# Kernel optimization log

Measured on AMD Instinct MI355X. Metric: run time of the kernel, lower is better.

The kernel has to match this reference:

```python
import jax, jax.numpy as jnp
import numpy as np

HIDDEN = 1024
HEADS = 16
HEAD_DIM = HIDDEN // HEADS


def setup_inputs() -> dict:
    key = jax.random.key(0)
    ks = jax.random.split(key, 12)
    B, S, D = 4, 2048, HIDDEN
    scale = 1.0 / np.sqrt(D)
    inp = {
        'q': jax.random.normal(ks[0], (B, S, D), jnp.float32),
        'k': jax.random.normal(ks[1], (B, S, D), jnp.float32),
        'v': jax.random.normal(ks[2], (B, S, D), jnp.float32),
        'Wq': jax.random.normal(ks[3], (D, D), jnp.float32) * scale,
        'bq': jnp.zeros((D,), jnp.float32),
        'Wk': jax.random.normal(ks[4], (D, D), jnp.float32) * scale,
        'bk': jnp.zeros((D,), jnp.float32),
        'Wv': jax.random.normal(ks[5], (D, D), jnp.float32) * scale,
        'bv': jnp.zeros((D,), jnp.float32),
        'Wo': jax.random.normal(ks[6], (D, D), jnp.float32) * scale,
        'bo': jnp.zeros((D,), jnp.float32),
    }
    return inp


def reference(q, k, v, Wq, bq, Wk, bk, Wv, bv, Wo, bo):
    B, S, D = q.shape
    H, Dh = HEADS, HEAD_DIM
    # QKV projections (weights stored as [in, out])
    Q = q @ Wq + bq
    K = k @ Wk + bk
    V = v @ Wv + bv
    # [B, H, S, Dh]
    Qh = Q.reshape(B, S, H, Dh).transpose(0, 2, 1, 3)
    Kh = K.reshape(B, S, H, Dh).transpose(0, 2, 1, 3)
    Vh = V.reshape(B, S, H, Dh).transpose(0, 2, 1, 3)
    # scaled dot-product attention, full [B,H,S,S] scores as in source
    scores = jnp.einsum('bhqd,bhkd->bhqk', Qh, Kh) / jnp.sqrt(jnp.float32(Dh))
    attn = jax.nn.softmax(scores, axis=-1)
    ctx = jnp.einsum('bhqk,bhkd->bhqd', attn, Vh)
    out = ctx.transpose(0, 2, 1, 3).reshape(B, S, D)
    return out @ Wo + bo
```

## Files before the change

kernel.cpp:

```cpp
#include <hip/hip_runtime.h>
#include <hip/hip_bf16.h>

#define HID 1024
#define NH 16
#define DH 64
#define NB 4
#define SQ 2048

typedef __bf16 bf16x8 __attribute__((ext_vector_type(8)));
typedef __bf16 bf16x2 __attribute__((ext_vector_type(2)));
typedef float f32x4 __attribute__((ext_vector_type(4)));
typedef float f32x16 __attribute__((ext_vector_type(16)));
typedef unsigned int u32x4 __attribute__((ext_vector_type(4)));

static __device__ __forceinline__ unsigned pkbf(float a, float b) {
  bf16x2 t; t[0] = (__bf16)a; t[1] = (__bf16)b;
  return __builtin_bit_cast(unsigned, t);
}

static __device__ __forceinline__ void gload16(const void* g, void* l) {
  __builtin_amdgcn_global_load_lds(
      (const __attribute__((address_space(1))) unsigned int*)g,
      (__attribute__((address_space(3))) unsigned int*)l, 16, 0, 0);
}

static __device__ __forceinline__ int xcd_swz(int lin, int nwg) {
  return (lin & 7) * (nwg >> 3) + (lin >> 3);
}

__global__ __launch_bounds__(256) void transpose_wf4_kernel(
    const float* __restrict__ Wq, const float* __restrict__ Wk,
    const float* __restrict__ Wv, const float* __restrict__ Wo,
    __bf16* __restrict__ Wcatf, __bf16* __restrict__ Wof) {
  const int which = blockIdx.z;
  const float* W = which == 0 ? Wq : (which == 1 ? Wk : (which == 2 ? Wv : Wo));
  __bf16* Wf = which == 3 ? Wof : Wcatf + (size_t)which * HID * HID;
  const int nblk = blockIdx.x, kt = blockIdx.y;
  const int tid = threadIdx.x, lane = tid & 63, wid = tid >> 6;
  const int fr = lane & 15, g = lane >> 4;
#pragma unroll
  for (int c = 0; c < 2; ++c) {
    const int wn_i = wid + c * 4;
    const int wn = wn_i >> 2, i = wn_i & 3;
    const int n = nblk * 128 + wn * 64 + i * 16 + fr;
    const int kb = kt * 32 + g * 8;
    bf16x8 v;
#pragma unroll
    for (int e = 0; e < 8; ++e)
      v[e] = (__bf16)W[(size_t)(kb + e) * HID + n];
    *reinterpret_cast<bf16x8*>(
        &Wf[(size_t)(nblk * 32 + kt) * 4096 + wn * 2048 + i * 512 + lane * 8]) = v;
  }
}

__global__ __launch_bounds__(256) void cvt_a_kernel(
    const float* __restrict__ q, const float* __restrict__ k,
    const float* __restrict__ v, __bf16* __restrict__ Abf) {
  const int which = blockIdx.y;
  const float* src = which == 0 ? q : (which == 1 ? k : v);
  __bf16* dst = Abf + (size_t)which * ((size_t)NB * SQ * HID);
  const size_t base = ((size_t)blockIdx.x * 256 + threadIdx.x) * 16;
  float4 f0 = *reinterpret_cast<const float4*>(src + base);
  float4 f1 = *reinterpret_cast<const float4*>(src + base + 4);
  float4 f2 = *reinterpret_cast<const float4*>(src + base + 8);
  float4 f3 = *reinterpret_cast<const float4*>(src + base + 12);
  u32x4 w0, w1;
  w0[0] = pkbf(f0.x, f0.y); w0[1] = pkbf(f0.z, f0.w);
  w0[2] = pkbf(f1.x, f1.y); w0[3] = pkbf(f1.z, f1.w);
  w1[0] = pkbf(f2.x, f2.y); w1[1] = pkbf(f2.z, f2.w);
  w1[2] = pkbf(f3.x, f3.y); w1[3] = pkbf(f3.z, f3.w);
  *reinterpret_cast<u32x4*>(dst + base) = w0;
  *reinterpret_cast<u32x4*>(dst + base + 8) = w1;
}

__global__ __launch_bounds__(256) void gemm_qkv_kernel(
    const __bf16* __restrict__ Abf, const __bf16* __restrict__ Wcatf,
    const float* __restrict__ bq, const float* __restrict__ bk,
    const float* __restrict__ bv, __bf16* __restrict__ Qh,
    __bf16* __restrict__ Kh, __bf16* __restrict__ Vt, float qscale) {
  const int K = HID;
  __shared__ __align__(16) char Asm[2][8192];
  const int tid = threadIdx.x;
  const int lane = tid & 63;
  const int wid = tid >> 6;
  const int wm = wid >> 1, wn = wid & 1;
  const int lin = blockIdx.x + 24 * blockIdx.y;
  const int work = xcd_swz(lin, 1536);
  const int seg = work >> 9;
  const int rem = work & 511;
  const int m0 = (rem >> 3) * 128;
  const int nblk = seg * 8 + (rem & 7);
  const int n0 = nblk * 128;
  const int fr = lane & 15, g = lane >> 4, kg = (lane >> 4) * 8;

  const __bf16* Ap = Abf + (size_t)seg * ((size_t)NB * SQ) * K;
  const __bf16* abf =
      Ap + (size_t)(m0 + wid * 32 + (lane >> 2)) * K + (lane & 3) * 8;
  const __bf16* wsrc = Wcatf + (size_t)nblk * 32 * 4096 + wn * 2048 + lane * 8;

  auto stageA = [&](int buf, int kt) {
    char* ab = &Asm[buf][0] + wid * 2048;
#pragma unroll
    for (int j = 0; j < 2; ++j)
      gload16(abf + (size_t)j * 16 * K + kt * 32, ab + j * 1024);
  };
  auto loadB = [&](int kt, bf16x8* br) {
    const __bf16* bp = wsrc + (size_t)kt * 4096;
#pragma unroll
    for (int i = 0; i < 4; ++i)
      br[i] = *reinterpret_cast<const bf16x8*>(bp + i * 512);
  };
  auto readA = [&](int buf, bf16x8* af) {
    const char* ac = &Asm[buf][0];
#pragma unroll
    for (int i = 0; i < 4; ++i)
      af[i] = *reinterpret_cast<const bf16x8*>(
          ac + (wm * 64 + i * 16 + fr) * 64 + kg * 2);
  };

  f32x4 acc[4][4] = {};
  const int NT = K / 32;
  bf16x8 bE[4], bO[4];
  stageA(0, 0);
  loadB(0, bE);
  __syncthreads();
  int cur = 0;
  for (int kt = 0; kt < NT; kt += 2) {
    stageA(cur ^ 1, kt + 1);
    loadB(kt + 1, bO);
    {
      bf16x8 af[4];
      readA(cur, af);
#pragma unroll
      for (int i = 0; i < 4; ++i)
#pragma unroll
        for (int j = 0; j < 4; ++j)
          acc[i][j] = __builtin_amdgcn_mfma_f32_16x16x32_bf16(
              af[i], bE[j], acc[i][j], 0, 0, 0);
    }
    __syncthreads();
    cur ^= 1;
    if (kt + 2 < NT) {
      stageA(cur ^ 1, kt + 2);
      loadB(kt + 2, bE);
    }
    {
      bf16x8 af[4];
      readA(cur, af);
#pragma unroll
      for (int i = 0; i < 4; ++i)
#pragma unroll
        for (int j = 0; j < 4; ++j)
          acc[i][j] = __builtin_amdgcn_mfma_f32_16x16x32_bf16(
              af[i], bO[j], acc[i][j], 0, 0, 0);
    }
    if (kt + 2 < NT) {
      __syncthreads();
      cur ^= 1;
    }
  }

  const float* bias = seg == 0 ? bq : (seg == 1 ? bk : bv);
  const float oscale = seg == 0 ? qscale : 1.f;
#pragma unroll
  for (int i = 0; i < 4; ++i) {
#pragma unroll
    for (int j = 0; j < 4; ++j) {
      const int n = n0 + wn * 64 + j * 16 + fr;
      const int nn = n & 1023;
      const float bn = bias[nn];
      const int h = nn >> 6, dh = nn & (DH - 1);
#pragma unroll
      for (int r = 0; r < 4; ++r) {
        const int m = m0 + wm * 64 + i * 16 + g * 4 + r;
        const float v = (acc[i][j][r] + bn) * oscale;
        const int b = m >> 11, s = m & (SQ - 1);
        if (seg == 0) {
          Qh[(((size_t)(b * NH + h) * SQ) + s) * DH + dh] = (__bf16)v;
        } else if (seg == 1) {
          const int kvt = s >> 5, ql = s & 31;
          const int ds = dh >> 4, hi = (dh >> 3) & 1, e = dh & 7;
          Kh[(size_t)(b * NH + h) * SQ * DH +
             (size_t)kvt * 2048 + ds * 512 + (hi * 32 + ql) * 8 + e] = (__bf16)v;
        } else {
          const int i64 = s >> 6, c16 = (s >> 4) & 3;
          const int hi = (s >> 2) & 1, e = (s & 3) + 4 * ((s >> 3) & 1);
          const int dblk = dh >> 5, ql = dh & 31;
          Vt[(size_t)(b * NH + h) * SQ * DH +
             (size_t)i64 * 4096 + dblk * 2048 + c16 * 512 +
             (hi * 32 + ql) * 8 + e] = (__bf16)v;
        }
      }
    }
  }
}

__global__ __launch_bounds__(256) void gemm_out_kernel(
    const __bf16* __restrict__ Ap, const __bf16* __restrict__ Wof,
    const float* __restrict__ bias, float* __restrict__ out,
    int M, int N, int K) {
  __shared__ __align__(16) char Asm[2][8192];
  const int tid = threadIdx.x;
  const int lane = tid & 63;
  const int wid = tid >> 6;
  const int wm = wid >> 1, wn = wid & 1;
  const int gx = N / 128;
  const int lin = blockIdx.x + gx * blockIdx.y;
  const int work = xcd_swz(lin, gx * (M / 128));
  const int m0 = (work / gx) * 128, nblk = work % gx, n0 = nblk * 128;
  const int fr = lane & 15, g = lane >> 4, kg = (lane >> 4) * 8;

  const __bf16* abf = Ap + (size_t)(m0 + wid * 32 + (lane >> 2)) * K + (lane & 3) * 8;
  const __bf16* wsrc = Wof + (size_t)nblk * 32 * 4096 + wn * 2048 + lane * 8;

  auto stageA = [&](int buf, int kt) {
    char* ab = &Asm[buf][0] + wid * 2048;
#pragma unroll
    for (int j = 0; j < 2; ++j)
      gload16(abf + (size_t)j * 16 * K + kt * 32, ab + j * 1024);
  };
  auto loadB = [&](int kt, bf16x8* br) {
    const __bf16* bp = wsrc + (size_t)kt * 4096;
#pragma unroll
    for (int i = 0; i < 4; ++i)
      br[i] = *reinterpret_cast<const bf16x8*>(bp + i * 512);
  };
  auto readA = [&](int buf, bf16x8* af) {
    const char* ac = &Asm[buf][0];
#pragma unroll
    for (int i = 0; i < 4; ++i)
      af[i] = *reinterpret_cast<const bf16x8*>(
          ac + (wm * 64 + i * 16 + fr) * 64 + kg * 2);
  };

  f32x4 acc[4][4] = {};
  const int NT = K / 32;
  bf16x8 bE[4], bO[4];
  stageA(0, 0);
  loadB(0, bE);
  __syncthreads();
  int cur = 0;
  for (int kt = 0; kt < NT; kt += 2) {
    stageA(cur ^ 1, kt + 1);
    loadB(kt + 1, bO);
    {
      bf16x8 af[4];
      readA(cur, af);
#pragma unroll
      for (int i = 0; i < 4; ++i)
#pragma unroll
        for (int j = 0; j < 4; ++j)
          acc[i][j] = __builtin_amdgcn_mfma_f32_16x16x32_bf16(
              af[i], bE[j], acc[i][j], 0, 0, 0);
    }
    __syncthreads();
    cur ^= 1;
    if (kt + 2 < NT) {
      stageA(cur ^ 1, kt + 2);
      loadB(kt + 2, bE);
    }
    {
      bf16x8 af[4];
      readA(cur, af);
#pragma unroll
      for (int i = 0; i < 4; ++i)
#pragma unroll
        for (int j = 0; j < 4; ++j)
          acc[i][j] = __builtin_amdgcn_mfma_f32_16x16x32_bf16(
              af[i], bO[j], acc[i][j], 0, 0, 0);
    }
    if (kt + 2 < NT) {
      __syncthreads();
      cur ^= 1;
    }
  }

#pragma unroll
  for (int i = 0; i < 4; ++i) {
#pragma unroll
    for (int j = 0; j < 4; ++j) {
      const int n = n0 + wn * 64 + j * 16 + fr;
      const float bn = bias[n];
#pragma unroll
      for (int r = 0; r < 4; ++r) {
        const int m = m0 + wm * 64 + i * 16 + g * 4 + r;
        out[(size_t)m * N + n] = acc[i][j][r] + bn;
      }
    }
  }
}

__global__ __launch_bounds__(256) void attn_kernel(
    const __bf16* __restrict__ Q, const __bf16* __restrict__ K,
    const __bf16* __restrict__ V, __bf16* __restrict__ ctx) {
  __shared__ float tb[4][32][33];
  const int tid = threadIdx.x, lane = tid & 63, wid = tid >> 6;
  const int lin = blockIdx.x + 16 * blockIdx.y;
  const int work = xcd_swz(lin, 16 * NB * NH);
  const int bh = work >> 4;
  const int q0 = (work & 15) * 128 + wid * 32;
  const int ql = lane & 31, hi = lane >> 5;
  const __bf16* Qb = Q + (size_t)bh * SQ * DH;
  const __bf16* Kf = K + (size_t)bh * SQ * DH;
  const __bf16* Vf = V + (size_t)bh * SQ * DH;

  bf16x8 qf[4];
#pragma unroll
  for (int ds = 0; ds < 4; ++ds)
    qf[ds] = *reinterpret_cast<const bf16x8*>(
        &Qb[(size_t)(q0 + ql) * DH + ds * 16 + hi * 8]);

  f32x16 ot0 = {}, ot1 = {};
  float l_run = 0.f;

  for (int kv0 = 0; kv0 < SQ; kv0 += 64) {
    const __bf16* Ka = Kf + (size_t)(kv0 >> 5) * 2048 + lane * 8;
    const __bf16* Kc = Ka + 2048;
    bf16x8 kfa0 = *reinterpret_cast<const bf16x8*>(Ka);
    bf16x8 kfa1 = *reinterpret_cast<const bf16x8*>(Ka + 512);
    bf16x8 kfa2 = *reinterpret_cast<const bf16x8*>(Ka + 1024);
    bf16x8 kfa3 = *reinterpret_cast<const bf16x8*>(Ka + 1536);
    bf16x8 kfb0 = *reinterpret_cast<const bf16x8*>(Kc);
    bf16x8 kfb1 = *reinterpret_cast<const bf16x8*>(Kc + 512);
    bf16x8 kfb2 = *reinterpret_cast<const bf16x8*>(Kc + 1024);
    bf16x8 kfb3 = *reinterpret_cast<const bf16x8*>(Kc + 1536);
    const __bf16* Vbase = Vf + (size_t)(kv0 >> 6) * 4096 + lane * 8;
    bf16x8 v00a = *reinterpret_cast<const bf16x8*>(Vbase);
    bf16x8 v01a = *reinterpret_cast<const bf16x8*>(Vbase + 512);
    bf16x8 v00b = *reinterpret_cast<const bf16x8*>(Vbase + 1024);
    bf16x8 v01b = *reinterpret_cast<const bf16x8*>(Vbase + 1536);
    bf16x8 v10a = *reinterpret_cast<const bf16x8*>(Vbase + 2048);
    bf16x8 v11a = *reinterpret_cast<const bf16x8*>(Vbase + 2560);
    bf16x8 v10b = *reinterpret_cast<const bf16x8*>(Vbase + 3072);
    bf16x8 v11b = *reinterpret_cast<const bf16x8*>(Vbase + 3584);

    f32x16 sa = {}, sb = {};
    __builtin_amdgcn_s_setprio(1);
    sa = __builtin_amdgcn_mfma_f32_32x32x16_bf16(kfa0, qf[0], sa, 0, 0, 0);
    sb = __builtin_amdgcn_mfma_f32_32x32x16_bf16(kfb0, qf[0], sb, 0, 0, 0);
    sa = __builtin_amdgcn_mfma_f32_32x32x16_bf16(kfa1, qf[1], sa, 0, 0, 0);
    sb = __builtin_amdgcn_mfma_f32_32x32x16_bf16(kfb1, qf[1], sb, 0, 0, 0);
    sa = __builtin_amdgcn_mfma_f32_32x32x16_bf16(kfa2, qf[2], sa, 0, 0, 0);
    sb = __builtin_amdgcn_mfma_f32_32x32x16_bf16(kfb2, qf[2], sb, 0, 0, 0);
    sa = __builtin_amdgcn_mfma_f32_32x32x16_bf16(kfa3, qf[3], sa, 0, 0, 0);
    sb = __builtin_amdgcn_mfma_f32_32x32x16_bf16(kfb3, qf[3], sb, 0, 0, 0);
    __builtin_amdgcn_s_setprio(0);

    float pa[16], pb_[16];
#pragma unroll
    for (int r = 0; r < 16; ++r) pa[r] = __builtin_amdgcn_exp2f(sa[r]);
#pragma unroll
    for (int r = 0; r < 16; ++r) pb_[r] = __builtin_amdgcn_exp2f(sb[r]);
    {
      float u0 = 0.f, u1 = 0.f, u2 = 0.f, u3 = 0.f;
#pragma unroll
      for (int r = 0; r < 4; ++r) {
        u0 += pa[r] + pa[r + 4];
        u1 += pa[r + 8] + pa[r + 12];
        u2 += pb_[r] + pb_[r + 4];
        u3 += pb_[r + 8] + pb_[r + 12];
      }
      l_run += (u0 + u1) + (u2 + u3);
    }
    unsigned ca[8], cb[8];
#pragma unroll
    for (int i = 0; i < 8; ++i) {
      ca[i] = pkbf(pa[2 * i], pa[2 * i + 1]);
      cb[i] = pkbf(pb_[2 * i], pb_[2 * i + 1]);
    }
    u32x4 WA0, WA1, WB0, WB1;
    WA0[0] = ca[0]; WA0[1] = ca[1]; WA0[2] = ca[2]; WA0[3] = ca[3];
    WA1[0] = ca[4]; WA1[1] = ca[5]; WA1[2] = ca[6]; WA1[3] = ca[7];
    WB0[0] = cb[0]; WB0[1] = cb[1]; WB0[2] = cb[2]; WB0[3] = cb[3];
    WB1[0] = cb[4]; WB1[1] = cb[5]; WB1[2] = cb[6]; WB1[3] = cb[7];
    bf16x8 pa0 = __builtin_bit_cast(bf16x8, WA0);
    bf16x8 pa1 = __builtin_bit_cast(bf16x8, WA1);
    bf16x8 pb0 = __builtin_bit_cast(bf16x8, WB0);
    bf16x8 pb1 = __builtin_bit_cast(bf16x8, WB1);
    __builtin_amdgcn_s_setprio(1);
    ot0 = __builtin_amdgcn_mfma_f32_32x32x16_bf16(v00a, pa0, ot0, 0, 0, 0);
    ot1 = __builtin_amdgcn_mfma_f32_32x32x16_bf16(v10a, pa0, ot1, 0, 0, 0);
    ot0 = __builtin_amdgcn_mfma_f32_32x32x16_bf16(v01a, pa1, ot0, 0, 0, 0);
    ot1 = __builtin_amdgcn_mfma_f32_32x32x16_bf16(v11a, pa1, ot1, 0, 0, 0);
    ot0 = __builtin_amdgcn_mfma_f32_32x32x16_bf16(v00b, pb0, ot0, 0, 0, 0);
    ot1 = __builtin_amdgcn_mfma_f32_32x32x16_bf16(v10b, pb0, ot1, 0, 0, 0);
    ot0 = __builtin_amdgcn_mfma_f32_32x32x16_bf16(v01b, pb1, ot0, 0, 0, 0);
    ot1 = __builtin_amdgcn_mfma_f32_32x32x16_bf16(v11b, pb1, ot1, 0, 0, 0);
    __builtin_amdgcn_s_setprio(0);
  }
  l_run += __shfl_xor(l_run, 32);
  const float inv = 1.f / l_run;

  const int qr = lane >> 1, hf = lane & 1;
  const int b = bh >> 4, h = bh & 15;
  __bf16* dstb = ctx + ((size_t)(b * SQ + q0 + qr)) * HID + h * 64 + hf * 16;
#pragma unroll
  for (int r = 0; r < 16; ++r)
    tb[wid][ql][(r & 3) + 8 * (r >> 2) + 4 * hi] = ot0[r] * inv;
  {
    unsigned wb[8];
#pragma unroll
    for (int i = 0; i < 8; ++i)
      wb[i] = pkbf(tb[wid][qr][hf * 16 + 2 * i], tb[wid][qr][hf * 16 + 2 * i + 1]);
    u32x4 W0, W1;
    W0[0] = wb[0]; W0[1] = wb[1]; W0[2] = wb[2]; W0[3] = wb[3];
    W1[0] = wb[4]; W1[1] = wb[5]; W1[2] = wb[6]; W1[3] = wb[7];
    *reinterpret_cast<u32x4*>(dstb) = W0;
    *reinterpret_cast<u32x4*>(dstb + 8) = W1;
  }
  __builtin_amdgcn_s_waitcnt(0);
#pragma unroll
  for (int r = 0; r < 16; ++r)
    tb[wid][ql][(r & 3) + 8 * (r >> 2) + 4 * hi] = ot1[r] * inv;
  {
    unsigned wb[8];
#pragma unroll
    for (int i = 0; i < 8; ++i)
      wb[i] = pkbf(tb[wid][qr][hf * 16 + 2 * i], tb[wid][qr][hf * 16 + 2 * i + 1]);
    u32x4 W0, W1;
    W0[0] = wb[0]; W0[1] = wb[1]; W0[2] = wb[2]; W0[3] = wb[3];
    W1[0] = wb[4]; W1[1] = wb[5]; W1[2] = wb[6]; W1[3] = wb[7];
    *reinterpret_cast<u32x4*>(dstb + 32) = W0;
    *reinterpret_cast<u32x4*>(dstb + 40) = W1;
  }
}

extern "C" void kernel_launch(void* const* d_in, const int* in_sizes, int n_in,
                              void* d_out, int out_size, void* d_ws, size_t ws_size,
                              hipStream_t stream) {
  const float* q  = (const float*)d_in[0];
  const float* k  = (const float*)d_in[1];
  const float* v  = (const float*)d_in[2];
  const float* Wq = (const float*)d_in[3];
  const float* bq = (const float*)d_in[4];
  const float* Wk = (const float*)d_in[5];
  const float* bk = (const float*)d_in[6];
  const float* Wv = (const float*)d_in[7];
  const float* bv = (const float*)d_in[8];
  const float* Wo = (const float*)d_in[9];
  const float* bo = (const float*)d_in[10];

  char* ws = (char*)d_ws;
  const size_t WSZ = (size_t)HID * HID * 2;
  const size_t QSZ = (size_t)NB * NH * SQ * DH * 2;
  __bf16* Wcatf = (__bf16*)(ws);
  __bf16* Wof  = (__bf16*)(ws + 3 * WSZ);
  __bf16* Qh   = (__bf16*)(ws + 4 * WSZ);
  __bf16* Kh   = (__bf16*)(ws + 4 * WSZ + QSZ);
  __bf16* Vt   = (__bf16*)(ws + 4 * WSZ + 2 * QSZ);
  __bf16* ctxb = (__bf16*)(ws + 4 * WSZ + 3 * QSZ);
  __bf16* Abf  = (__bf16*)(ws + 4 * WSZ + 4 * QSZ);

  const int M = NB * SQ;
  const float qscale = 0.125f * 1.44269504088896f;

  cvt_a_kernel<<<dim3((size_t)NB * SQ * HID / 4096, 3), 256, 0, stream>>>(
      q, k, v, Abf);

  transpose_wf4_kernel<<<dim3(8, 32, 4), 256, 0, stream>>>(
      Wq, Wk, Wv, Wo, Wcatf, Wof);

  gemm_qkv_kernel<<<dim3(24, 64), 256, 0, stream>>>(
      Abf, Wcatf, bq, bk, bv, Qh, Kh, Vt, qscale);

  attn_kernel<<<dim3(SQ / 128, NB * NH), 256, 0, stream>>>(Qh, Kh, Vt, ctxb);

  gemm_out_kernel<<<dim3(HID / 128, M / 128), 256, 0, stream>>>(
      ctxb, Wof, bo, (float*)d_out, M, HID, HID);
}
```

Baseline: 236.5 us.

## Stage GEMM weight tiles through LDS via async loads; restructure input cast

Both projection GEMMs now copy B (weight) tiles into a double-buffered LDS area with global_load_lds, alongside the A tiles. Each wave previously loaded its B fragments straight into registers, so the two waves sharing a column fetched the same data twice. Now each weight tile is fetched once per block and shared, at the cost of doubling LDS use per block and adding LDS reads. The fp32-to-bf16 cast kernel is also reworked so each thread handles four strided float4 chunks for better coalescing.

```diff
diff --git a/kernel.cpp b/kernel.cpp
--- a/kernel.cpp
+++ b/kernel.cpp
@@ -59,18 +59,16 @@
   const int which = blockIdx.y;
   const float* src = which == 0 ? q : (which == 1 ? k : v);
   __bf16* dst = Abf + (size_t)which * ((size_t)NB * SQ * HID);
-  const size_t base = ((size_t)blockIdx.x * 256 + threadIdx.x) * 16;
-  float4 f0 = *reinterpret_cast<const float4*>(src + base);
-  float4 f1 = *reinterpret_cast<const float4*>(src + base + 4);
-  float4 f2 = *reinterpret_cast<const float4*>(src + base + 8);
-  float4 f3 = *reinterpret_cast<const float4*>(src + base + 12);
-  u32x4 w0, w1;
-  w0[0] = pkbf(f0.x, f0.y); w0[1] = pkbf(f0.z, f0.w);
-  w0[2] = pkbf(f1.x, f1.y); w0[3] = pkbf(f1.z, f1.w);
-  w1[0] = pkbf(f2.x, f2.y); w1[1] = pkbf(f2.z, f2.w);
-  w1[2] = pkbf(f3.x, f3.y); w1[3] = pkbf(f3.z, f3.w);
-  *reinterpret_cast<u32x4*>(dst + base) = w0;
-  *reinterpret_cast<u32x4*>(dst + base + 8) = w1;
+  const size_t blockbase = (size_t)blockIdx.x * 4096;
+#pragma unroll
+  for (int j = 0; j < 4; ++j) {
+    const size_t idx = blockbase + j * 1024 + (size_t)threadIdx.x * 4;
+    float4 f = *reinterpret_cast<const float4*>(src + idx);
+    uint2 w;
+    w.x = pkbf(f.x, f.y);
+    w.y = pkbf(f.z, f.w);
+    *reinterpret_cast<uint2*>(dst + idx) = w;
+  }
 }
 
 __global__ __launch_bounds__(256) void gemm_qkv_kernel(
@@ -80,6 +78,7 @@
     __bf16* __restrict__ Kh, __bf16* __restrict__ Vt, float qscale) {
   const int K = HID;
   __shared__ __align__(16) char Asm[2][8192];
+  __shared__ __align__(16) char Bsm[2][8192];
   const int tid = threadIdx.x;
   const int lane = tid & 63;
   const int wid = tid >> 6;
@@ -96,19 +95,17 @@
   const __bf16* Ap = Abf + (size_t)seg * ((size_t)NB * SQ) * K;
   const __bf16* abf =
       Ap + (size_t)(m0 + wid * 32 + (lane >> 2)) * K + (lane & 3) * 8;
-  const __bf16* wsrc = Wcatf + (size_t)nblk * 32 * 4096 + wn * 2048 + lane * 8;
-
-  auto stageA = [&](int buf, int kt) {
+  const __bf16* wb = Wcatf + (size_t)nblk * 32 * 4096 + wid * 512 + lane * 8;
+
+  auto stage = [&](int buf, int kt) {
     char* ab = &Asm[buf][0] + wid * 2048;
 #pragma unroll
     for (int j = 0; j < 2; ++j)
       gload16(abf + (size_t)j * 16 * K + kt * 32, ab + j * 1024);
-  };
-  auto loadB = [&](int kt, bf16x8* br) {
-    const __bf16* bp = wsrc + (size_t)kt * 4096;
-#pragma unroll
-    for (int i = 0; i < 4; ++i)
-      br[i] = *reinterpret_cast<const bf16x8*>(bp + i * 512);
+    char* bb = &Bsm[buf][0] + wid * 1024;
+#pragma unroll
+    for (int j = 0; j < 2; ++j)
+      gload16(wb + (size_t)kt * 4096 + j * 2048, bb + j * 4096);
   };
   auto readA = [&](int buf, bf16x8* af) {
     const char* ac = &Asm[buf][0];
@@ -117,47 +114,44 @@
       af[i] = *reinterpret_cast<const bf16x8*>(
           ac + (wm * 64 + i * 16 + fr) * 64 + kg * 2);
   };
+  auto readB = [&](int buf, bf16x8* bf_) {
+    const char* bc = &Bsm[buf][0] + wn * 4096 + lane * 16;
+#pragma unroll
+    for (int i = 0; i < 4; ++i)
+      bf_[i] = *reinterpret_cast<const bf16x8*>(bc + i * 1024);
+  };
 
   f32x4 acc[4][4] = {};
   const int NT = K / 32;
-  bf16x8 bE[4], bO[4];
-  stageA(0, 0);
-  loadB(0, bE);
+  stage(0, 0);
   __syncthreads();
-  int cur = 0;
   for (int kt = 0; kt < NT; kt += 2) {
-    stageA(cur ^ 1, kt + 1);
-    loadB(kt + 1, bO);
+    stage(1, kt + 1);
     {
-      bf16x8 af[4];
-      readA(cur, af);
+      bf16x8 af[4], bf_[4];
+      readA(0, af);
+      readB(0, bf_);
 #pragma unroll
       for (int i = 0; i < 4; ++i)
 #pragma unroll
         for (int j = 0; j < 4; ++j)
           acc[i][j] = __builtin_amdgcn_mfma_f32_16x16x32_bf16(
-              af[i], bE[j], acc[i][j], 0, 0, 0);
+              af[i], bf_[j], acc[i][j], 0, 0, 0);
     }
     __syncthreads();
-    cur ^= 1;
-    if (kt + 2 < NT) {
-      stageA(cur ^ 1, kt + 2);
-      loadB(kt + 2, bE);
-    }
+    if (kt + 2 < NT) stage(0, kt + 2);
     {
-      bf16x8 af[4];
-      readA(cur, af);
+      bf16x8 af[4], bf_[4];
+      readA(1, af);
+      readB(1, bf_);
 #pragma unroll
       for (int i = 0; i < 4; ++i)
 #pragma unroll
         for (int j = 0; j < 4; ++j)
           acc[i][j] = __builtin_amdgcn_mfma_f32_16x16x32_bf16(
-              af[i], bO[j], acc[i][j], 0, 0, 0);
-    }
-    if (kt + 2 < NT) {
-      __syncthreads();
-      cur ^= 1;
-    }
+              af[i], bf_[j], acc[i][j], 0, 0, 0);
+    }
+    if (kt + 2 < NT) __syncthreads();
   }
 
   const float* bias = seg == 0 ? bq : (seg == 1 ? bk : bv);
@@ -200,6 +194,7 @@
     const float* __restrict__ bias, float* __restrict__ out,
     int M, int N, int K) {
   __shared__ __align__(16) char Asm[2][8192];
+  __shared__ __align__(16) char Bsm[2][8192];
   const int tid = threadIdx.x;
   const int lane = tid & 63;
   const int wid = tid >> 6;
@@ -211,19 +206,17 @@
   const int fr = lane & 15, g = lane >> 4, kg = (lane >> 4) * 8;
 
   const __bf16* abf = Ap + (size_t)(m0 + wid * 32 + (lane >> 2)) * K + (lane & 3) * 8;
-  const __bf16* wsrc = Wof + (size_t)nblk * 32 * 4096 + wn * 2048 + lane * 8;
-
-  auto stageA = [&](int buf, int kt) {
+  const __bf16* wb = Wof + (size_t)nblk * 32 * 4096 + wid * 512 + lane * 8;
+
+  auto stage = [&](int buf, int kt) {
     char* ab = &Asm[buf][0] + wid * 2048;
 #pragma unroll
     for (int j = 0; j < 2; ++j)
       gload16(abf + (size_t)j * 16 * K + kt * 32, ab + j * 1024);
-  };
-  auto loadB = [&](int kt, bf16x8* br) {
-    const __bf16* bp = wsrc + (size_t)kt * 4096;
-#pragma unroll
-    for (int i = 0; i < 4; ++i)
-      br[i] = *reinterpret_cast<const bf16x8*>(bp + i * 512);
+    char* bb = &Bsm[buf][0] + wid * 1024;
+#pragma unroll
+    for (int j = 0; j < 2; ++j)
+      gload16(wb + (size_t)kt * 4096 + j * 2048, bb + j * 4096);
   };
   auto readA = [&](int buf, bf16x8* af) {
     const char* ac = &Asm[buf][0];
@@ -232,47 +225,44 @@
       af[i] = *reinterpret_cast<const bf16x8*>(
           ac + (wm * 64 + i * 16 + fr) * 64 + kg * 2);
   };
+  auto readB = [&](int buf, bf16x8* bf_) {
+    const char* bc = &Bsm[buf][0] + wn * 4096 + lane * 16;
+#pragma unroll
+    for (int i = 0; i < 4; ++i)
+      bf_[i] = *reinterpret_cast<const bf16x8*>(bc + i * 1024);
+  };
 
   f32x4 acc[4][4] = {};
   const int NT = K / 32;
-  bf16x8 bE[4], bO[4];
-  stageA(0, 0);
-  loadB(0, bE);
+  stage(0, 0);
   __syncthreads();
-  int cur = 0;
   for (int kt = 0; kt < NT; kt += 2) {
-    stageA(cur ^ 1, kt + 1);
-    loadB(kt + 1, bO);
+    stage(1, kt + 1);
     {
-      bf16x8 af[4];
-      readA(cur, af);
+      bf16x8 af[4], bf_[4];
+      readA(0, af);
+      readB(0, bf_);
 #pragma unroll
       for (int i = 0; i < 4; ++i)
 #pragma unroll
         for (int j = 0; j < 4; ++j)
           acc[i][j] = __builtin_amdgcn_mfma_f32_16x16x32_bf16(
-              af[i], bE[j], acc[i][j], 0, 0, 0);
+              af[i], bf_[j], acc[i][j], 0, 0, 0);
     }
     __syncthreads();
-    cur ^= 1;
-    if (kt + 2 < NT) {
-      stageA(cur ^ 1, kt + 2);
-      loadB(kt + 2, bE);
-    }
+    if (kt + 2 < NT) stage(0, kt + 2);
     {
-      bf16x8 af[4];
-      readA(cur, af);
+      bf16x8 af[4], bf_[4];
+      readA(1, af);
+      readB(1, bf_);
 #pragma unroll
       for (int i = 0; i < 4; ++i)
 #pragma unroll
         for (int j = 0; j < 4; ++j)
           acc[i][j] = __builtin_amdgcn_mfma_f32_16x16x32_bf16(
-              af[i], bO[j], acc[i][j], 0, 0, 0);
-    }
-    if (kt + 2 < NT) {
-      __syncthreads();
-      cur ^= 1;
-    }
+              af[i], bf_[j], acc[i][j], 0, 0, 0);
+    }
+    if (kt + 2 < NT) __syncthreads();
   }
 
 #pragma unroll
```

Result: slower. 244.6 us (+3.4%).
